# Performance work log

Hardware: AMD Instinct MI355X
Metric: run time of the kernel (lower is better)

Reference implementation:

```python
import jax, jax.numpy as jnp
import numpy as np

N_NODES = 50000
N_EDGES = 600000
IN_SIZE = 128
HIDDEN = 256
OUT_SIZE = 128


def _xavier(key, shape):
    fan_out, fan_in = shape
    lim = jnp.sqrt(6.0 / (fan_in + fan_out))
    return jax.random.uniform(key, shape, jnp.float32, -lim, lim)


def setup_inputs() -> dict:
    key = jax.random.key(0)
    ks = jax.random.split(key, 8)
    feat = jax.random.normal(ks[0], (N_NODES, IN_SIZE), jnp.float32)
    edge_index = jax.random.randint(ks[1], (2, N_EDGES), 0, N_NODES, jnp.int32)
    return {
        "feat": feat,
        "edge_index": edge_index,
        "W1l": _xavier(ks[2], (HIDDEN, IN_SIZE)),
        "b1": jnp.zeros((HIDDEN,), jnp.float32),
        "W1r": _xavier(ks[3], (HIDDEN, IN_SIZE)),
        "W2l": _xavier(ks[4], (OUT_SIZE, HIDDEN)),
        "b2": jnp.zeros((OUT_SIZE,), jnp.float32),
        "W2r": _xavier(ks[5], (OUT_SIZE, HIDDEN)),
        "Wfc": _xavier(ks[6], (2, OUT_SIZE)),
        "bfc": jnp.zeros((2,), jnp.float32),
    }


def _sage_conv(x, src, dst, Wl, bl, Wr):
    # mean-aggregate neighbor features: messages x[src] scattered to dst
    agg = jax.ops.segment_sum(x[src], dst, num_segments=N_NODES)
    cnt = jax.ops.segment_sum(jnp.ones((src.shape[0],), x.dtype), dst,
                              num_segments=N_NODES)
    agg = agg / jnp.maximum(cnt, 1.0)[:, None]
    out = agg @ Wl.T + bl + x @ Wr.T
    # F.normalize(p=2, dim=-1), eps=1e-12
    norm = jnp.maximum(jnp.linalg.norm(out, axis=-1, keepdims=True), 1e-12)
    return out / norm


def reference(feat, edge_index, W1l, b1, W1r, W2l, b2, W2r, Wfc, bfc):
    src, dst = edge_index[0], edge_index[1]
    h = _sage_conv(feat, src, dst, W1l, b1, W1r)
    h = jax.nn.relu(h)
    h = _sage_conv(h, src, dst, W2l, b2, W2r)
    logits = h @ Wfc.T + bfc
    return jax.nn.softmax(logits, axis=-1)
```

## Files before the change

kernel.cpp:

```cpp
#include <hip/hip_runtime.h>
#include <hip/hip_fp8.h>
#include <math.h>

#define N_NODES  50000
#define N_EDGES  600000
#define CAP      64
#define POISON   0xAAAAAAAAu
#define CSTRIDE  16

typedef __attribute__((ext_vector_type(8))) short bf16x8;
typedef __attribute__((ext_vector_type(4))) float f32x4;
typedef unsigned int uint32;

__device__ __forceinline__ unsigned short f2bf(float x) {
  uint32 u = __builtin_bit_cast(uint32, x);
  u += 0x7FFFu + ((u >> 16) & 1u);
  return (unsigned short)(u >> 16);
}
__device__ __forceinline__ float bf2f(uint32 lo16) {
  return __builtin_bit_cast(float, lo16 << 16);
}
__device__ __forceinline__ uint32 pack2(float a, float b) {
  return (uint32)f2bf(a) | ((uint32)f2bf(b) << 16);
}
__device__ __forceinline__ unsigned char f2q(float x) {
  __hip_fp8_e4m3 q(x);
  return __builtin_bit_cast(unsigned char, q);
}
__device__ __forceinline__ float q2f(uint32 b) {
  return (float)__builtin_bit_cast(__hip_fp8_e4m3, (unsigned char)(b & 0xffu));
}

#define FCHUNK      8192
#define NCHUNK      ((N_EDGES + FCHUNK - 1) / FCHUNK)
#define FILL_BLOCKS (NCHUNK * 8)
#define PREP_FEAT_BLOCKS 6250
#define PREP_W_BLOCKS    256
__global__ void k_prepfill(const float* __restrict__ feat, unsigned short* __restrict__ featb,
                           unsigned short* __restrict__ feat8,
                           const float* __restrict__ W1l, const float* __restrict__ W1r,
                           unsigned short* __restrict__ Wc1,
                           const float* __restrict__ W2l, const float* __restrict__ W2r,
                           unsigned short* __restrict__ Wc2,
                           const int* __restrict__ src, const int* __restrict__ dst,
                           uint32* __restrict__ cnt, int* __restrict__ col) {
  const int bid = blockIdx.x, t = threadIdx.x;
  if (bid < FILL_BLOCKS) {
    const int part = bid & 7;
    const int chunk = bid >> 3;
    const int e0 = chunk * FCHUNK;
    const int eend = min(e0 + FCHUNK, N_EDGES);
    #pragma unroll 1
    for (int base = e0 + t; base < eend; base += 256 * 8) {
      int dd[8];
      #pragma unroll
      for (int k = 0; k < 8; ++k) {
        int e = base + k * 256;
        dd[k] = (e < eend) ? dst[e] : (part ^ 1);
      }
      #pragma unroll
      for (int k = 0; k < 8; ++k) {
        if ((dd[k] & 7) == part) {
          int e = base + k * 256;
          int s = src[e];
          uint32 p = atomicAdd(&cnt[(size_t)dd[k] * CSTRIDE], 1u) - POISON;
          if (p < CAP) col[(size_t)dd[k] * CAP + p] = s;
        }
      }
    }
  } else if (bid < FILL_BLOCKS + PREP_FEAT_BLOCKS) {
    int i = (bid - FILL_BLOCKS) * 256 + t;
    float4 v = ((const float4*)feat)[i];
    uint2 fb;
    fb.x = pack2(v.x, v.y);
    fb.y = pack2(v.z, v.w);
    ((uint2*)featb)[i] = fb;
    uint32 f8 = (uint32)f2q(v.x) | ((uint32)f2q(v.y) << 8) |
                ((uint32)f2q(v.z) << 16) | ((uint32)f2q(v.w) << 24);
    ((uint32*)feat8)[i] = f8;
  } else if (bid < FILL_BLOCKS + PREP_FEAT_BLOCKS + PREP_W_BLOCKS) {
    int id = (bid - FILL_BLOCKS - PREP_FEAT_BLOCKS) * 256 + t;
    int n = id >> 8, k = id & 255;
    float v = (k < 128) ? W1l[n * 128 + k] : W1r[n * 128 + (k - 128)];
    Wc1[id] = f2bf(v);
  } else {
    int id = (bid - FILL_BLOCKS - PREP_FEAT_BLOCKS - PREP_W_BLOCKS) * 256 + t;
    int n = id >> 8, k = id & 255;
    float v = (n < 128) ? W2l[n * 256 + k] : W2r[(n - 128) * 256 + k];
    Wc2[id] = f2bf(v);
  }
}
#define PREPFILL_BLOCKS (FILL_BLOCKS + PREP_FEAT_BLOCKS + 2 * PREP_W_BLOCKS)

__device__ __forceinline__ int read_deg(const uint32* __restrict__ cnt, int n) {
  uint32 d = cnt[(size_t)n * CSTRIDE] - POISON;
  return (int)(d < (uint32)CAP ? d : (uint32)CAP);
}

__device__ __forceinline__ void gather16_u2(const uint2* __restrict__ base,
                                            const int* __restrict__ col,
                                            int rs, int dg, int sl,
                                            float4& lo, float4& hi) {
  int idx[16];
  #pragma unroll
  for (int q = 0; q < 16; ++q) idx[q] = col[rs + q];
  uint2 v[16];
  #pragma unroll
  for (int q = 0; q < 16; ++q) { v[q].x = 0u; v[q].y = 0u; }
  #pragma unroll
  for (int q = 0; q < 16; ++q)
    if (q < dg) v[q] = base[(size_t)idx[q] * 16 + sl];
  float4 al[4], ah[4];
  #pragma unroll
  for (int q = 0; q < 4; ++q) {
    al[q] = (float4){0.f, 0.f, 0.f, 0.f};
    ah[q] = (float4){0.f, 0.f, 0.f, 0.f};
  }
  #pragma unroll
  for (int q = 0; q < 16; ++q) {
    int a = q & 3;
    al[a].x += q2f(v[q].x);       al[a].y += q2f(v[q].x >> 8);
    al[a].z += q2f(v[q].x >> 16); al[a].w += q2f(v[q].x >> 24);
    ah[a].x += q2f(v[q].y);       ah[a].y += q2f(v[q].y >> 8);
    ah[a].z += q2f(v[q].y >> 16); ah[a].w += q2f(v[q].y >> 24);
  }
  #pragma unroll 1
  for (int j = 16; j < dg; j += 8) {
    int tix[8];
    #pragma unroll
    for (int q = 0; q < 8; ++q) tix[q] = col[rs + j + q];
    uint2 tv2[8];
    #pragma unroll
    for (int q = 0; q < 8; ++q) { tv2[q].x = 0u; tv2[q].y = 0u; }
    #pragma unroll
    for (int q = 0; q < 8; ++q)
      if (j + q < dg) tv2[q] = base[(size_t)tix[q] * 16 + sl];
    #pragma unroll
    for (int q = 0; q < 8; ++q) {
      int a = q & 3;
      al[a].x += q2f(tv2[q].x);       al[a].y += q2f(tv2[q].x >> 8);
      al[a].z += q2f(tv2[q].x >> 16); al[a].w += q2f(tv2[q].x >> 24);
      ah[a].x += q2f(tv2[q].y);       ah[a].y += q2f(tv2[q].y >> 8);
      ah[a].z += q2f(tv2[q].y >> 16); ah[a].w += q2f(tv2[q].y >> 24);
    }
  }
  float4 s02l, s13l, s02h, s13h;
  s02l.x = al[0].x + al[2].x; s02l.y = al[0].y + al[2].y; s02l.z = al[0].z + al[2].z; s02l.w = al[0].w + al[2].w;
  s13l.x = al[1].x + al[3].x; s13l.y = al[1].y + al[3].y; s13l.z = al[1].z + al[3].z; s13l.w = al[1].w + al[3].w;
  s02h.x = ah[0].x + ah[2].x; s02h.y = ah[0].y + ah[2].y; s02h.z = ah[0].z + ah[2].z; s02h.w = ah[0].w + ah[2].w;
  s13h.x = ah[1].x + ah[3].x; s13h.y = ah[1].y + ah[3].y; s13h.z = ah[1].z + ah[3].z; s13h.w = ah[1].w + ah[3].w;
  lo.x = s02l.x + s13l.x; lo.y = s02l.y + s13l.y; lo.z = s02l.z + s13l.z; lo.w = s02l.w + s13l.w;
  hi.x = s02h.x + s13h.x; hi.y = s02h.y + s13h.y; hi.z = s02h.z + s13h.z; hi.w = s02h.w + s13h.w;
}

__global__ void k_agg1(const unsigned short* __restrict__ feat8, const uint32* __restrict__ cnt,
                       const int* __restrict__ col, unsigned short* __restrict__ agg) {
  int t = threadIdx.x;
  int sl = t & 15;
  int n = blockIdx.x * 16 + (t >> 4);
  int dg = read_deg(cnt, n);
  float4 lo, hi;
  gather16_u2((const uint2*)feat8, col, n * CAP, dg, sl, lo, hi);
  float inv = 1.0f / fmaxf((float)dg, 1.0f);
  uint4 o;
  o.x = pack2(lo.x * inv, lo.y * inv);
  o.y = pack2(lo.z * inv, lo.w * inv);
  o.z = pack2(hi.x * inv, hi.y * inv);
  o.w = pack2(hi.z * inv, hi.w * inv);
  ((uint4*)agg)[(size_t)n * 16 + sl] = o;
}

#define H1S 264
__global__ __launch_bounds__(256, 2) void k_gemm12(
    const unsigned short* __restrict__ A0, const unsigned short* __restrict__ A1,
    const unsigned short* __restrict__ W1, const float* __restrict__ bias,
    const unsigned short* __restrict__ W2,
    unsigned char* __restrict__ Tl8, unsigned short* __restrict__ Yr) {
  __shared__ unsigned short Ws[2048 * 8];
  __shared__ unsigned short h1S[64 * H1S];
  __shared__ float red[4][32];
  const int t = threadIdx.x, lane = t & 63, w = t >> 6;
  const int mi = lane & 15, quad = lane >> 4;
  const int rowHalf = w >> 1, colHalf = w & 1;
  const int m0 = blockIdx.x * 64 + rowHalf * 32;
  const int col0 = colHalf * 128;
  const int rowA0 = min(m0 + mi, N_NODES - 1);
  const int rowA1 = min(m0 + 16 + mi, N_NODES - 1);

  f32x4 acc[2][8];
  #pragma unroll
  for (int rt = 0; rt < 2; ++rt)
    #pragma unroll
    for (int nt = 0; nt < 8; ++nt) acc[rt][nt] = (f32x4){0.f, 0.f, 0.f, 0.f};

  #pragma unroll
  for (int ks = 0; ks < 4; ++ks) {
    if (ks) __syncthreads();
    #pragma unroll
    for (int i = 0; i < 8; ++i) {
      int ch0 = (w * 8 + i) * 64;
      int qp = ch0 >> 8, n0 = ch0 & 255;
      const unsigned short* gp = W1 + (size_t)(n0 + lane) * 256 + ks * 64 + qp * 8;
      unsigned short* lp = Ws + (size_t)ch0 * 8;
      __builtin_amdgcn_global_load_lds(
          (const __attribute__((address_space(1))) void*)gp,
          (__attribute__((address_space(3))) void*)lp, 16, 0, 0);
    }
    const unsigned short* Asrc = (ks < 2) ? A0 : A1;
    const int koff = (ks & 1) * 64;
    bf16x8 af[2][2];
    af[0][0] = *(const bf16x8*)(Asrc + (size_t)rowA0 * 128 + koff + quad * 8);
    af[0][1] = *(const bf16x8*)(Asrc + (size_t)rowA0 * 128 + koff + 32 + quad * 8);
    af[1][0] = *(const bf16x8*)(Asrc + (size_t)rowA1 * 128 + koff + quad * 8);
    af[1][1] = *(const bf16x8*)(Asrc + (size_t)rowA1 * 128 + koff + 32 + quad * 8);
    __syncthreads();
    #pragma unroll
    for (int kc = 0; kc < 2; ++kc)
      #pragma unroll
      for (int nt = 0; nt < 8; ++nt) {
        bf16x8 b = *(const bf16x8*)(Ws + ((size_t)(kc * 4 + quad) * 256 + col0 + nt * 16 + mi) * 8);
        acc[0][nt] = __builtin_amdgcn_mfma_f32_16x16x32_bf16(af[0][kc], b, acc[0][nt], 0, 0, 0);
        acc[1][nt] = __builtin_amdgcn_mfma_f32_16x16x32_bf16(af[1][kc], b, acc[1][nt], 0, 0, 0);
      }
  }

  float ss[2][4] = {};
  #pragma unroll
  for (int nt = 0; nt < 8; ++nt) {
    float bv = bias[col0 + nt * 16 + mi];
    #pragma unroll
    for (int rt = 0; rt < 2; ++rt)
      #pragma unroll
      for (int r = 0; r < 4; ++r) {
        float v = acc[rt][nt][r] + bv;
        acc[rt][nt][r] = v;
        ss[rt][r] += v * v;
      }
  }
  #pragma unroll
  for (int rt = 0; rt < 2; ++rt)
    #pragma unroll
    for (int r = 0; r < 4; ++r) {
      float s = ss[rt][r];
      s += __shfl_xor(s, 1, 64);
      s += __shfl_xor(s, 2, 64);
      s += __shfl_xor(s, 4, 64);
      s += __shfl_xor(s, 8, 64);
      ss[rt][r] = s;
    }
  __syncthreads();
  if (mi == 0) {
    #pragma unroll
    for (int rt = 0; rt < 2; ++rt)
      #pragma unroll
      for (int r = 0; r < 4; ++r)
        red[w][rt * 16 + quad * 4 + r] = ss[rt][r];
  }
  __syncthreads();
  #pragma unroll
  for (int rt = 0; rt < 2; ++rt)
    #pragma unroll
    for (int r = 0; r < 4; ++r) {
      float full = ss[rt][r] + red[w ^ 1][rt * 16 + quad * 4 + r];
      ss[rt][r] = 1.0f / fmaxf(sqrtf(full), 1e-12f);
    }
  #pragma unroll
  for (int rt = 0; rt < 2; ++rt)
    #pragma unroll
    for (int r = 0; r < 4; ++r) {
      int rl = rowHalf * 32 + rt * 16 + quad * 4 + r;
      #pragma unroll
      for (int nt = 0; nt < 8; ++nt)
        h1S[(size_t)rl * H1S + col0 + nt * 16 + mi] =
            f2bf(fmaxf(acc[rt][nt][r] * ss[rt][r], 0.f));
    }
  __syncthreads();

  #pragma unroll
  for (int rt = 0; rt < 2; ++rt)
    #pragma unroll
    for (int nt = 0; nt < 8; ++nt) acc[rt][nt] = (f32x4){0.f, 0.f, 0.f, 0.f};

  const int rl0 = rowHalf * 32 + mi;
  const int rl1 = rowHalf * 32 + 16 + mi;
  #pragma unroll
  for (int ks = 0; ks < 4; ++ks) {
    if (ks) __syncthreads();
    #pragma unroll
    for (int i = 0; i < 8; ++i) {
      int ch0 = (w * 8 + i) * 64;
      int qp = ch0 >> 8, n0 = ch0 & 255;
      const unsigned short* gp = W2 + (size_t)(n0 + lane) * 256 + ks * 64 + qp * 8;
      unsigned short* lp = Ws + (size_t)ch0 * 8;
      __builtin_amdgcn_global_load_lds(
          (const __attribute__((address_space(1))) void*)gp,
          (__attribute__((address_space(3))) void*)lp, 16, 0, 0);
    }
    bf16x8 af[2][2];
    af[0][0] = *(const bf16x8*)(h1S + (size_t)rl0 * H1S + ks * 64 + quad * 8);
    af[0][1] = *(const bf16x8*)(h1S + (size_t)rl0 * H1S + ks * 64 + 32 + quad * 8);
    af[1][0] = *(const bf16x8*)(h1S + (size_t)rl1 * H1S + ks * 64 + quad * 8);
    af[1][1] = *(const bf16x8*)(h1S + (size_t)rl1 * H1S + ks * 64 + 32 + quad * 8);
    __syncthreads();
    #pragma unroll
    for (int kc = 0; kc < 2; ++kc)
      #pragma unroll
      for (int nt = 0; nt < 8; ++nt) {
        bf16x8 b = *(const bf16x8*)(Ws + ((size_t)(kc * 4 + quad) * 256 + col0 + nt * 16 + mi) * 8);
        acc[0][nt] = __builtin_amdgcn_mfma_f32_16x16x32_bf16(af[0][kc], b, acc[0][nt], 0, 0, 0);
        acc[1][nt] = __builtin_amdgcn_mfma_f32_16x16x32_bf16(af[1][kc], b, acc[1][nt], 0, 0, 0);
      }
  }

  if (colHalf == 0) {
    #pragma unroll
    for (int rt = 0; rt < 2; ++rt)
      #pragma unroll
      for (int r = 0; r < 4; ++r) {
        int row = m0 + rt * 16 + quad * 4 + r;
        if (row < N_NODES) {
          #pragma unroll
          for (int nt = 0; nt < 8; ++nt)
            Tl8[(size_t)row * 128 + nt * 16 + mi] = f2q(acc[rt][nt][r]);
        }
      }
  } else {
    #pragma unroll
    for (int rt = 0; rt < 2; ++rt)
      #pragma unroll
      for (int r = 0; r < 4; ++r) {
        int row = m0 + rt * 16 + quad * 4 + r;
        if (row < N_NODES) {
          #pragma unroll
          for (int nt = 0; nt < 8; ++nt)
            Yr[(size_t)row * 128 + nt * 16 + mi] = f2bf(acc[rt][nt][r]);
        }
      }
  }
}

__global__ void k_final(const unsigned char* __restrict__ Tl8, const unsigned short* __restrict__ Tr,
                        const uint32* __restrict__ cnt, const int* __restrict__ col,
                        const float* __restrict__ b2, const float* __restrict__ Wfc,
                        const float* __restrict__ bfc, float* __restrict__ out) {
  int t = threadIdx.x;
  int sl = t & 15;
  int n = blockIdx.x * 16 + (t >> 4);
  int dg = read_deg(cnt, n);
  float4 lo, hi;
  gather16_u2((const uint2*)Tl8, col, n * CAP, dg, sl, lo, hi);
  uint4 tv = ((const uint4*)Tr)[(size_t)n * 16 + sl];
  float4 bb0 = ((const float4*)b2)[sl * 2];
  float4 bb1 = ((const float4*)b2)[sl * 2 + 1];
  float4 w00 = ((const float4*)Wfc)[sl * 2];
  float4 w01 = ((const float4*)Wfc)[sl * 2 + 1];
  float4 w10 = ((const float4*)Wfc)[32 + sl * 2];
  float4 w11 = ((const float4*)Wfc)[32 + sl * 2 + 1];
  float inv = 1.0f / fmaxf((float)dg, 1.0f);
  float h0 = lo.x * inv + bf2f(tv.x & 0xffffu) + bb0.x;
  float h1 = lo.y * inv + bf2f(tv.x >> 16)     + bb0.y;
  float h2 = lo.z * inv + bf2f(tv.y & 0xffffu) + bb0.z;
  float h3 = lo.w * inv + bf2f(tv.y >> 16)     + bb0.w;
  float h4 = hi.x * inv + bf2f(tv.z & 0xffffu) + bb1.x;
  float h5 = hi.y * inv + bf2f(tv.z >> 16)     + bb1.y;
  float h6 = hi.z * inv + bf2f(tv.w & 0xffffu) + bb1.z;
  float h7 = hi.w * inv + bf2f(tv.w >> 16)     + bb1.w;
  float ss = h0 * h0 + h1 * h1 + h2 * h2 + h3 * h3 +
             h4 * h4 + h5 * h5 + h6 * h6 + h7 * h7;
  ss += __shfl_xor(ss, 1, 64);
  ss += __shfl_xor(ss, 2, 64);
  ss += __shfl_xor(ss, 4, 64);
  ss += __shfl_xor(ss, 8, 64);
  float iv = 1.0f / fmaxf(sqrtf(ss), 1e-12f);
  float p0 = h0 * w00.x + h1 * w00.y + h2 * w00.z + h3 * w00.w +
             h4 * w01.x + h5 * w01.y + h6 * w01.z + h7 * w01.w;
  float p1 = h0 * w10.x + h1 * w10.y + h2 * w10.z + h3 * w10.w +
             h4 * w11.x + h5 * w11.y + h6 * w11.z + h7 * w11.w;
  p0 *= iv; p1 *= iv;
  #pragma unroll
  for (int m = 1; m < 16; m <<= 1) {
    p0 += __shfl_xor(p0, m, 64);
    p1 += __shfl_xor(p1, m, 64);
  }
  if (sl == 0) {
    float l0 = p0 + bfc[0], l1 = p1 + bfc[1];
    float mx = fmaxf(l0, l1);
    float e0 = expf(l0 - mx), e1 = expf(l1 - mx);
    float sden = 1.0f / (e0 + e1);
    out[(size_t)n * 2 + 0] = e0 * sden;
    out[(size_t)n * 2 + 1] = e1 * sden;
  }
}

extern "C" void kernel_launch(void* const* d_in, const int* in_sizes, int n_in,
                              void* d_out, int out_size, void* d_ws, size_t ws_size,
                              hipStream_t stream) {
  const float* feat = (const float*)d_in[0];
  const int* eidx = (const int*)d_in[1];
  const int* src = eidx;
  const int* dst = eidx + N_EDGES;
  const float* W1l = (const float*)d_in[2];
  const float* b1  = (const float*)d_in[3];
  const float* W1r = (const float*)d_in[4];
  const float* W2l = (const float*)d_in[5];
  const float* b2  = (const float*)d_in[6];
  const float* W2r = (const float*)d_in[7];
  const float* Wfc = (const float*)d_in[8];
  const float* bfc = (const float*)d_in[9];
  float* out = (float*)d_out;

  uint32* cnt    = (uint32*)d_ws;
  int* col       = (int*)(cnt + 50000 * CSTRIDE);
  unsigned short* featb = (unsigned short*)(col + 3200064);
  unsigned short* feat8 = featb + 6400000;
  unsigned short* agg1b = feat8 + 3200000;
  unsigned short* h1b   = agg1b + 6400000;
  unsigned char*  Tl8   = (unsigned char*)(h1b + 12800000);
  unsigned short* Trb   = (unsigned short*)(Tl8 + 6400000);
  unsigned short* Wc1   = Trb + 6400000;
  unsigned short* Wc2   = Wc1 + 65536;

  k_prepfill<<<PREPFILL_BLOCKS, 256, 0, stream>>>(feat, featb, feat8, W1l, W1r, Wc1,
                                                  W2l, W2r, Wc2, src, dst, cnt, col);

  k_agg1<<<N_NODES / 16, 256, 0, stream>>>(feat8, cnt, col, agg1b);
  k_gemm12<<<(N_NODES + 63) / 64, 256, 0, stream>>>(agg1b, featb, Wc1, b1, Wc2, Tl8, Trb);
  k_final<<<N_NODES / 16, 256, 0, stream>>>(Tl8, Trb, cnt, col, b2, Wfc, bfc, out);
}
```

Before: 210.2 us.

## Flatten edge fill to one-pass vectorized atomics and pre-tile weights for coalesced LDS loads

The CSR fill drops the 8-way partitioned multi-pass scan over edges. Each thread now loads four dst/src pairs with int4 loads and does its atomics directly, so the dst array is read once instead of eight times. The weight prep now stores the bf16 weights in a k-chunk-major tiled layout, so the GEMM's global_load_lds reads are contiguous 16-byte chunks rather than strided rows. The cost is losing the partition's locality of atomics per destination group, which may raise atomic contention or scatter.

```diff
diff --git a/kernel.cpp b/kernel.cpp
--- a/kernel.cpp
+++ b/kernel.cpp
@@ -31,9 +31,8 @@
   return (float)__builtin_bit_cast(__hip_fp8_e4m3, (unsigned char)(b & 0xffu));
 }
 
-#define FCHUNK      8192
-#define NCHUNK      ((N_EDGES + FCHUNK - 1) / FCHUNK)
-#define FILL_BLOCKS (NCHUNK * 8)
+#define FILL_THREADS     (N_EDGES / 4)
+#define FILL_BLOCKS      ((FILL_THREADS + 255) / 256)
 #define PREP_FEAT_BLOCKS 6250
 #define PREP_W_BLOCKS    256
 __global__ void k_prepfill(const float* __restrict__ feat, unsigned short* __restrict__ featb,
@@ -46,27 +45,18 @@
                            uint32* __restrict__ cnt, int* __restrict__ col) {
   const int bid = blockIdx.x, t = threadIdx.x;
   if (bid < FILL_BLOCKS) {
-    const int part = bid & 7;
-    const int chunk = bid >> 3;
-    const int e0 = chunk * FCHUNK;
-    const int eend = min(e0 + FCHUNK, N_EDGES);
-    #pragma unroll 1
-    for (int base = e0 + t; base < eend; base += 256 * 8) {
-      int dd[8];
-      #pragma unroll
-      for (int k = 0; k < 8; ++k) {
-        int e = base + k * 256;
-        dd[k] = (e < eend) ? dst[e] : (part ^ 1);
-      }
-      #pragma unroll
-      for (int k = 0; k < 8; ++k) {
-        if ((dd[k] & 7) == part) {
-          int e = base + k * 256;
-          int s = src[e];
-          uint32 p = atomicAdd(&cnt[(size_t)dd[k] * CSTRIDE], 1u) - POISON;
-          if (p < CAP) col[(size_t)dd[k] * CAP + p] = s;
-        }
-      }
+    int i = bid * 256 + t;
+    if (i < FILL_THREADS) {
+      int4 d4 = ((const int4*)dst)[i];
+      int4 s4 = ((const int4*)src)[i];
+      uint32 p0 = atomicAdd(&cnt[(size_t)d4.x * CSTRIDE], 1u) - POISON;
+      uint32 p1 = atomicAdd(&cnt[(size_t)d4.y * CSTRIDE], 1u) - POISON;
+      uint32 p2 = atomicAdd(&cnt[(size_t)d4.z * CSTRIDE], 1u) - POISON;
+      uint32 p3 = atomicAdd(&cnt[(size_t)d4.w * CSTRIDE], 1u) - POISON;
+      if (p0 < CAP) col[(size_t)d4.x * CAP + p0] = s4.x;
+      if (p1 < CAP) col[(size_t)d4.y * CAP + p1] = s4.y;
+      if (p2 < CAP) col[(size_t)d4.z * CAP + p2] = s4.z;
+      if (p3 < CAP) col[(size_t)d4.w * CAP + p3] = s4.w;
     }
   } else if (bid < FILL_BLOCKS + PREP_FEAT_BLOCKS) {
     int i = (bid - FILL_BLOCKS) * 256 + t;
@@ -82,12 +72,12 @@
     int id = (bid - FILL_BLOCKS - PREP_FEAT_BLOCKS) * 256 + t;
     int n = id >> 8, k = id & 255;
     float v = (k < 128) ? W1l[n * 128 + k] : W1r[n * 128 + (k - 128)];
-    Wc1[id] = f2bf(v);
+    Wc1[(((k >> 3) * 256 + n) << 3) + (k & 7)] = f2bf(v);
   } else {
     int id = (bid - FILL_BLOCKS - PREP_FEAT_BLOCKS - PREP_W_BLOCKS) * 256 + t;
     int n = id >> 8, k = id & 255;
     float v = (n < 128) ? W2l[n * 256 + k] : W2r[(n - 128) * 256 + k];
-    Wc2[id] = f2bf(v);
+    Wc2[(((k >> 3) * 256 + n) << 3) + (k & 7)] = f2bf(v);
   }
 }
 #define PREPFILL_BLOCKS (FILL_BLOCKS + PREP_FEAT_BLOCKS + 2 * PREP_W_BLOCKS)
@@ -199,8 +189,7 @@
     #pragma unroll
     for (int i = 0; i < 8; ++i) {
       int ch0 = (w * 8 + i) * 64;
-      int qp = ch0 >> 8, n0 = ch0 & 255;
-      const unsigned short* gp = W1 + (size_t)(n0 + lane) * 256 + ks * 64 + qp * 8;
+      const unsigned short* gp = W1 + (size_t)(ks * 2048 + ch0 + lane) * 8;
       unsigned short* lp = Ws + (size_t)ch0 * 8;
       __builtin_amdgcn_global_load_lds(
           (const __attribute__((address_space(1))) void*)gp,
@@ -289,8 +278,7 @@
     #pragma unroll
     for (int i = 0; i < 8; ++i) {
       int ch0 = (w * 8 + i) * 64;
-      int qp = ch0 >> 8, n0 = ch0 & 255;
-      const unsigned short* gp = W2 + (size_t)(n0 + lane) * 256 + ks * 64 + qp * 8;
+      const unsigned short* gp = W2 + (size_t)(ks * 2048 + ch0 + lane) * 8;
       unsigned short* lp = Ws + (size_t)ch0 * 8;
       __builtin_amdgcn_global_load_lds(
           (const __attribute__((address_space(1))) void*)gp,
```

New measurement: 189.8 us, median of 2. -9.7%, faster.
